# Kernel tuning notes

Measured on AMD Instinct MI355X. Metric: run time of the kernel, lower is better.

The kernel has to match this reference:

```python
import jax, jax.numpy as jnp
import numpy as np

CUTOFF = 1.0  # nm
KE = 138.96   # Coulomb constant conversion factor used by the module


def physnet_attenuation(r, cutoff=CUTOFF):
    # PhysNet smooth switching function: 1 - 6u^5 + 15u^4 - 10u^3 for u<1, else 0
    u = r / cutoff
    phi = 1.0 - 6.0 * u**5 + 15.0 * u**4 - 10.0 * u**3
    return jnp.where(u < 1.0, phi, 0.0)


def setup_inputs() -> dict:
    key = jax.random.key(0)
    k1, k2, k3, k4 = jax.random.split(key, 4)
    N = 262144          # total atoms
    P = 16777216        # total pairs (~64 neighbors/atom)
    S = 1024            # number of systems
    pair_idx = jax.random.randint(k1, (2, P), 0, N, dtype=jnp.int32)
    # distances in (0.05, 1.25) nm; 2*d straddles the cutoff so both branches of chi_r are exercised
    d_ij = (jax.random.uniform(k2, (P, 1), dtype=jnp.float32) * 1.2 + 0.05)
    charge = jax.random.normal(k3, (N, 1), dtype=jnp.float32) * 0.3
    sys_idx = jnp.sort(jax.random.randint(k4, (N,), 0, S, dtype=jnp.int32))
    return {
        "electrostatic_pair_indices": pair_idx,
        "electrostatic_d_ij": d_ij,
        "per_atom_charge": charge,
        "atomic_subsystem_indices": sys_idx,
        "num_systems": S,
    }


def reference(electrostatic_pair_indices, electrostatic_d_ij, per_atom_charge,
              atomic_subsystem_indices, num_systems):
    idx_i = electrostatic_pair_indices[0]
    idx_j = electrostatic_pair_indices[1]
    # unique-pair mask (static shapes: zero out instead of filtering)
    mask = idx_i < idx_j
    d = electrostatic_d_ij[:, 0]                       # [P]
    q = per_atom_charge[:, 0]                          # [N]
    phi_2r = physnet_attenuation(2.0 * d)
    chi_r = phi_2r / jnp.sqrt(d * d + 1.0) + (1.0 - phi_2r) / d
    e_pair = q[idx_i] * q[idx_j] * chi_r               # [P]
    e_pair = jnp.where(mask, e_pair, 0.0)
    seg = atomic_subsystem_indices[idx_i]              # system of each pair
    per_system = jax.ops.segment_sum(e_pair, seg, num_segments=num_systems)
    return (per_system * KE)[:, None]                  # [S, 1]
```

## Files before the change

### kernel.cpp

```cpp
#include <hip/hip_runtime.h>

typedef int   v4i __attribute__((ext_vector_type(4)));
typedef float v4f __attribute__((ext_vector_type(4)));

#define S_SYS    1024
#define KE_CONST 138.96f
#define BLOCKS   1024
#define THREADS  512
#define NWAVE    (THREADS / 64)

__global__ __launch_bounds__(256) void pack_kernel(const float* __restrict__ q,
                                                   const int* __restrict__ sys,
                                                   float2* __restrict__ packed,
                                                   float* __restrict__ out, int N) {
    int i = blockIdx.x * blockDim.x + threadIdx.x;
    if (i < N) {
        float2 v;
        v.x = q[i];
        v.y = __int_as_float(sys[i]);
        packed[i] = v;
    }
    if (i < S_SYS) out[i] = 0.0f;
}

__global__ __launch_bounds__(THREADS, 4) void pair_kernel(const v4i* __restrict__ idx_i4,
                                                          const v4i* __restrict__ idx_j4,
                                                          const v4f* __restrict__ d4,
                                                          const float2* __restrict__ packed,
                                                          float* __restrict__ out,
                                                          int P4) {
    __shared__ float acc[NWAVE][S_SYS];
    const int tid  = threadIdx.x;
    const int wave = tid >> 6;
    const int lane = tid & 63;
    for (int t = tid; t < NWAVE * S_SYS; t += THREADS) ((float*)acc)[t] = 0.0f;
    __syncthreads();

    const int stride = gridDim.x * blockDim.x;
    for (int p = blockIdx.x * blockDim.x + tid; p < P4; p += 2 * stride) {
        const int p2 = p + stride;
        const bool has2 = (p2 < P4);

        v4i vi0 = __builtin_nontemporal_load(&idx_i4[p]);
        v4i vj0 = __builtin_nontemporal_load(&idx_j4[p]);
        v4f vd0 = __builtin_nontemporal_load(&d4[p]);
        v4i vi1 = {0, 0, 0, 0};
        v4i vj1 = {0, 0, 0, 0};
        v4f vd1 = {1.f, 1.f, 1.f, 1.f};
        if (has2) {
            vi1 = __builtin_nontemporal_load(&idx_i4[p2]);
            vj1 = __builtin_nontemporal_load(&idx_j4[p2]);
            vd1 = __builtin_nontemporal_load(&d4[p2]);
        }

        int   ii[8], jj[8];
        float dd[8];
#pragma unroll
        for (int k = 0; k < 4; ++k) { ii[k] = vi0[k];     jj[k] = vj0[k];     dd[k] = vd0[k]; }
#pragma unroll
        for (int k = 0; k < 4; ++k) { ii[4 + k] = vi1[k]; jj[4 + k] = vj1[k]; dd[4 + k] = vd1[k]; }

        bool act[8];
        int  gi[8], gj[8];
#pragma unroll
        for (int k = 0; k < 8; ++k) {
            act[k] = ii[k] < jj[k];
            gi[k]  = act[k] ? ii[k] : 0;
            gj[k]  = act[k] ? jj[k] : 0;
        }
        float2 pi[8];
        float  qj[8];
#pragma unroll
        for (int k = 0; k < 8; ++k) {
            pi[k] = packed[gi[k]];
            qj[k] = packed[gj[k]].x;
        }

#pragma unroll
        for (int k = 0; k < 8; ++k) {
            float d   = dd[k];
            float u   = 2.0f * d;
            float phi = 0.0f;
            if (u < 1.0f) {
                float u3 = u * u * u;
                phi = 1.0f - u3 * (10.0f + u * (6.0f * u - 15.0f));
            }
            float rcp = __builtin_amdgcn_rcpf(d);
            float chi = rcp + phi * (__builtin_amdgcn_rsqf(d * d + 1.0f) - rcp);
            float e   = pi[k].x * qj[k] * chi;
            float es  = act[k] ? e : 0.0f;
            int   bin = act[k] ? __float_as_int(pi[k].y) : lane;
            atomicAdd(&acc[wave][bin], es);
        }
    }
    __syncthreads();

    for (int s = tid; s < S_SYS; s += THREADS) {
        float v = 0.0f;
#pragma unroll
        for (int w = 0; w < NWAVE; ++w) v += acc[w][s];
        atomicAdd(&out[s], KE_CONST * v);
    }
}

extern "C" void kernel_launch(void* const* d_in, const int* in_sizes, int n_in,
                              void* d_out, int out_size, void* d_ws, size_t ws_size,
                              hipStream_t stream) {
    const int*   pair = (const int*)d_in[0];
    const float* d_ij = (const float*)d_in[1];
    const float* q    = (const float*)d_in[2];
    const int*   sys  = (const int*)d_in[3];
    const int P = in_sizes[1];
    const int N = in_sizes[2];
    float* out = (float*)d_out;

    float2* packed = (float2*)d_ws;

    pack_kernel<<<(N + 255) / 256, 256, 0, stream>>>(q, sys, packed, out, N);

    pair_kernel<<<BLOCKS, THREADS, 0, stream>>>(
        (const v4i*)pair, (const v4i*)(pair + P), (const v4f*)d_ij,
        packed, out, P / 4);
}
```

Before: 296.5 us.

## Software-pipeline streaming pair loads and predicate LDS atomics on active pairs

Restructures the grid-stride loop so the next iteration's index and distance vectors are loaded before the current iteration's gathers and math. This hides global load latency behind computation, and addresses are clamped so the prefetch needs no branch. It also makes the attenuation select branchless, adds a scheduling barrier after the gathers, and skips LDS atomics for inactive pairs instead of sending zeros to per-lane dummy bins. Costs include more live registers for the prefetched vectors, which may hurt occupancy at 4 blocks per CU, and a divergent branch around the atomics.

```diff
diff --git a/kernel.cpp b/kernel.cpp
--- a/kernel.cpp
+++ b/kernel.cpp
@@ -32,42 +32,47 @@
     __shared__ float acc[NWAVE][S_SYS];
     const int tid  = threadIdx.x;
     const int wave = tid >> 6;
-    const int lane = tid & 63;
     for (int t = tid; t < NWAVE * S_SYS; t += THREADS) ((float*)acc)[t] = 0.0f;
     __syncthreads();
 
     const int stride = gridDim.x * blockDim.x;
-    for (int p = blockIdx.x * blockDim.x + tid; p < P4; p += 2 * stride) {
-        const int p2 = p + stride;
-        const bool has2 = (p2 < P4);
+    const int step   = 2 * stride;
+    int p = blockIdx.x * blockDim.x + tid;
 
-        v4i vi0 = __builtin_nontemporal_load(&idx_i4[p]);
-        v4i vj0 = __builtin_nontemporal_load(&idx_j4[p]);
-        v4f vd0 = __builtin_nontemporal_load(&d4[p]);
-        v4i vi1 = {0, 0, 0, 0};
-        v4i vj1 = {0, 0, 0, 0};
-        v4f vd1 = {1.f, 1.f, 1.f, 1.f};
-        if (has2) {
-            vi1 = __builtin_nontemporal_load(&idx_i4[p2]);
-            vj1 = __builtin_nontemporal_load(&idx_j4[p2]);
-            vd1 = __builtin_nontemporal_load(&d4[p2]);
-        }
+    int a0 = p          < P4 ? p          : P4 - 1;
+    int b0 = p + stride < P4 ? p + stride : P4 - 1;
+    v4i vi0 = __builtin_nontemporal_load(&idx_i4[a0]);
+    v4i vj0 = __builtin_nontemporal_load(&idx_j4[a0]);
+    v4f vd0 = __builtin_nontemporal_load(&d4[a0]);
+    v4i vi1 = __builtin_nontemporal_load(&idx_i4[b0]);
+    v4i vj1 = __builtin_nontemporal_load(&idx_j4[b0]);
+    v4f vd1 = __builtin_nontemporal_load(&d4[b0]);
 
-        int   ii[8], jj[8];
-        float dd[8];
-#pragma unroll
-        for (int k = 0; k < 4; ++k) { ii[k] = vi0[k];     jj[k] = vj0[k];     dd[k] = vd0[k]; }
-#pragma unroll
-        for (int k = 0; k < 4; ++k) { ii[4 + k] = vi1[k]; jj[4 + k] = vj1[k]; dd[4 + k] = vd1[k]; }
+    while (p < P4) {
+        const int  pn = p + step;
+        const bool v1 = (p + stride) < P4;
+
+        int an = pn          < P4 ? pn          : P4 - 1;
+        int bn = pn + stride < P4 ? pn + stride : P4 - 1;
+        v4i nvi0 = __builtin_nontemporal_load(&idx_i4[an]);
+        v4i nvj0 = __builtin_nontemporal_load(&idx_j4[an]);
+        v4f nvd0 = __builtin_nontemporal_load(&d4[an]);
+        v4i nvi1 = __builtin_nontemporal_load(&idx_i4[bn]);
+        v4i nvj1 = __builtin_nontemporal_load(&idx_j4[bn]);
+        v4f nvd1 = __builtin_nontemporal_load(&d4[bn]);
 
         bool act[8];
         int  gi[8], gj[8];
 #pragma unroll
         for (int k = 0; k < 8; ++k) {
-            act[k] = ii[k] < jj[k];
-            gi[k]  = act[k] ? ii[k] : 0;
-            gj[k]  = act[k] ? jj[k] : 0;
+            int i  = (k < 4) ? vi0[k] : vi1[k - 4];
+            int j  = (k < 4) ? vj0[k] : vj1[k - 4];
+            bool a = (i < j) && ((k < 4) || v1);
+            act[k] = a;
+            gi[k]  = a ? i : 0;
+            gj[k]  = a ? j : 0;
         }
+
         float2 pi[8];
         float  qj[8];
 #pragma unroll
@@ -75,23 +80,23 @@
             pi[k] = packed[gi[k]];
             qj[k] = packed[gj[k]].x;
         }
+        __builtin_amdgcn_sched_barrier(0);
 
 #pragma unroll
         for (int k = 0; k < 8; ++k) {
-            float d   = dd[k];
+            float d   = (k < 4) ? vd0[k] : vd1[k - 4];
             float u   = 2.0f * d;
-            float phi = 0.0f;
-            if (u < 1.0f) {
-                float u3 = u * u * u;
-                phi = 1.0f - u3 * (10.0f + u * (6.0f * u - 15.0f));
-            }
+            float u3  = u * u * u;
+            float phi = (u < 1.0f) ? 1.0f - u3 * (10.0f + u * (6.0f * u - 15.0f)) : 0.0f;
             float rcp = __builtin_amdgcn_rcpf(d);
             float chi = rcp + phi * (__builtin_amdgcn_rsqf(d * d + 1.0f) - rcp);
             float e   = pi[k].x * qj[k] * chi;
-            float es  = act[k] ? e : 0.0f;
-            int   bin = act[k] ? __float_as_int(pi[k].y) : lane;
-            atomicAdd(&acc[wave][bin], es);
+            if (act[k]) atomicAdd(&acc[wave][__float_as_int(pi[k].y)], e);
         }
+
+        vi0 = nvi0; vj0 = nvj0; vd0 = nvd0;
+        vi1 = nvi1; vj1 = nvj1; vd1 = nvd1;
+        p = pn;
     }
     __syncthreads();
 
```

Measured after the change: 288.0 us (median of 2 runs). 1.03x faster.
